# Kernel tuning notes

Measured on AMD Instinct MI355X. Metric: run time of the kernel, lower is better.

## Reference

```python
import jax, jax.numpy as jnp
import numpy as np

N_NODES = 20000
N_EDGES = 320000
F_IN = 256
HID = 256
N_CLS = 5


def _glorot(key, shape):
    lim = np.sqrt(6.0 / (shape[0] + shape[1]))
    return jax.random.uniform(key, shape, jnp.float32, -lim, lim)


def setup_inputs() -> dict:
    key = jax.random.key(0)
    ks = jax.random.split(key, 12)
    x1 = jax.random.normal(ks[0], (N_NODES, F_IN), jnp.float32)
    x2 = jax.random.normal(ks[1], (N_NODES, F_IN), jnp.float32)
    ei1 = jax.random.randint(ks[2], (2, N_EDGES), 0, N_NODES, jnp.int64 if jax.config.jax_enable_x64 else jnp.int32)
    ei2 = jax.random.randint(ks[3], (2, N_EDGES), 0, N_NODES, jnp.int64 if jax.config.jax_enable_x64 else jnp.int32)
    params = {
        'W1': _glorot(ks[4], (F_IN, HID)), 'b1': jnp.zeros((HID,), jnp.float32),
        'W2': _glorot(ks[5], (HID, HID)), 'b2': jnp.zeros((HID,), jnp.float32),
        'W3': _glorot(ks[6], (HID, HID)), 'b3': jnp.zeros((HID,), jnp.float32),
        'Wl': _glorot(ks[7], (HID, N_CLS)), 'bl': jnp.zeros((N_CLS,), jnp.float32),
    }
    return {'x1': x1, 'edge_index1': ei1, 'x2': x2, 'edge_index2': ei2, **params}


def gcn_conv(x, edge_index, W, b):
    # PyG GCNConv: add self-loops, symmetric normalization D^-1/2 (A+I) D^-1/2 (X W) + b
    N = x.shape[0]
    src, dst = edge_index[0], edge_index[1]
    deg = jax.ops.segment_sum(jnp.ones(src.shape[0], x.dtype), dst, num_segments=N) + 1.0
    dinv = jax.lax.rsqrt(deg)  # [N]
    xw = x @ W                 # [N, H]
    coef = (dinv[src] * dinv[dst])[:, None]  # per-edge norm
    agg = jax.ops.segment_sum(xw[src] * coef, dst, num_segments=N)
    agg = agg + xw * (dinv * dinv)[:, None]  # self-loop term
    return agg + b


def _branch(x, ei, W1, b1, W2, b2, W3, b3):
    # dropout is identity in eval mode
    h = jax.nn.relu(gcn_conv(x, ei, W1, b1))
    h = jax.nn.relu(gcn_conv(h, ei, W2, b2))
    return gcn_conv(h, ei, W3, b3)


def reference(x1, edge_index1, x2, edge_index2, W1, b1, W2, b2, W3, b3, Wl, bl):
    h1 = _branch(x1, edge_index1, W1, b1, W2, b2, W3, b3)
    h2 = _branch(x2, edge_index2, W1, b1, W2, b2, W3, b3)
    h = jnp.concatenate([h1, h2], axis=0)          # [2N, H]
    pooled = jnp.mean(h, axis=0, keepdims=True)    # batch is all zeros -> single mean pool
    return pooled @ Wl + bl                        # [1, num_classes]
```

## Files before the change

### kernel.cpp

```cpp
#include <hip/hip_runtime.h>
#include <hip/hip_bf16.h>

#define N_NODES 20000
#define N_EDGES 320000
#define HID 256
#define NQ 5000
#define NCHUNK 64

typedef __attribute__((ext_vector_type(8))) short bf16x8;
typedef __attribute__((ext_vector_type(4))) float f32x4;
typedef __attribute__((ext_vector_type(8))) unsigned short us8;

__device__ __forceinline__ float bf2f(ushort u) {
  union { unsigned int i; float f; } v; v.i = ((unsigned int)u) << 16; return v.f;
}
__device__ __forceinline__ ushort f2bf(float f) {
  union { float f; unsigned int i; } v; v.f = f;
  unsigned int r = v.i + 0x7FFFu + ((v.i >> 16) & 1u);
  return (ushort)(r >> 16);
}

__global__ void init_detect_kernel(int* cnt0, int* cnt1, float* t0, float* t1,
                                   const void* x1, const void* ei1, int* flags) {
  if (blockIdx.x == gridDim.x - 1) {
    __shared__ int cnt_wild, cnt_oddnz;
    if (threadIdx.x == 0) { cnt_wild = 0; cnt_oddnz = 0; }
    __syncthreads();
    const ushort* xu = (const ushort*)x1;
    int wild = 0;
#pragma unroll
    for (int k = 0; k < 4; k++) {
      ushort u = xu[threadIdx.x * 4 + k];
      int ex = (u >> 7) & 0xFF;
      if (ex >= 0x90) wild++;
    }
    if (wild) atomicAdd(&cnt_wild, wild);
    const int* ii = (const int*)ei1;
    if (ii[threadIdx.x * 2 + 1] != 0) atomicAdd(&cnt_oddnz, 1);
    __syncthreads();
    if (threadIdx.x == 0) {
      flags[0] = (cnt_wild > 64) ? 1 : 0;
      flags[1] = (cnt_oddnz < 8) ? 1 : 0;
    }
    return;
  }
  int i = blockIdx.x * blockDim.x + threadIdx.x;
  if (i < N_NODES) { cnt0[i] = 0; cnt1[i] = 0; t0[i] = 0.f; t1[i] = 0.f; }
}

__global__ __launch_bounds__(1024) void count_rank_kernel(
    const void* e0, const void* e1, int* cnt0, int* cnt1,
    int* rank0, int* rank1, const int* flags) {
  int b = blockIdx.y;
  const void* e = b ? e1 : e0;
  int* cnt = b ? cnt1 : cnt0;
  int* rank = b ? rank1 : rank0;
  int chunk = blockIdx.x >> 2;
  int lo = (blockIdx.x & 3) * NQ;
  int ebeg = chunk * (N_EDGES / NCHUNK);
  int eend = ebeg + (N_EDGES / NCHUNK);
  __shared__ int hist[NQ];
  __shared__ int base[NQ];
  for (int k = threadIdx.x; k < NQ; k += 1024) hist[k] = 0;
  __syncthreads();
  bool w64 = flags[1] != 0;
  const int* d32 = (const int*)e + N_EDGES;
  const long long* d64 = (const long long*)e + N_EDGES;
  for (int i = ebeg + threadIdx.x; i < eend; i += 1024) {
    int d = w64 ? (int)d64[i] : d32[i];
    unsigned q = (unsigned)(d - lo);
    if (q < NQ) atomicAdd(&hist[q], 1);
  }
  __syncthreads();
  for (int k = threadIdx.x; k < NQ; k += 1024) {
    int h = hist[k];
    if (h) base[k] = atomicAdd(&cnt[lo + k], h);
    hist[k] = 0;
  }
  __syncthreads();
  for (int i = ebeg + threadIdx.x; i < eend; i += 1024) {
    int d = w64 ? (int)d64[i] : d32[i];
    unsigned q = (unsigned)(d - lo);
    if (q < NQ) rank[i] = base[q] + atomicAdd(&hist[q], 1);
  }
}

__global__ __launch_bounds__(1024) void scan_kernel(const int* cnt0, const int* cnt1,
                                                    int* rp0, int* rp1,
                                                    float* dinv0, float* dinv1) {
  const int* cnt = blockIdx.x ? cnt1 : cnt0;
  int* rp = blockIdx.x ? rp1 : rp0;
  float* dinv = blockIdx.x ? dinv1 : dinv0;
  __shared__ int sd[1024];
  int tid = threadIdx.x;
  int base = tid * 20;
  int pref[20];
  int run = 0;
#pragma unroll
  for (int k = 0; k < 20; k++) {
    int i = base + k;
    int c = (i < N_NODES) ? cnt[i] : 0;
    if (i < N_NODES) dinv[i] = rsqrtf((float)c + 1.0f);
    run += c;
    pref[k] = run;
  }
  sd[tid] = run;
  __syncthreads();
  for (int off = 1; off < 1024; off <<= 1) {
    int v = (tid >= off) ? sd[tid - off] : 0;
    __syncthreads();
    sd[tid] += v;
    __syncthreads();
  }
  int offset = sd[tid] - run;
  if (tid == 0) rp[0] = 0;
#pragma unroll
  for (int k = 0; k < 20; k++) {
    int i = base + k;
    if (i < N_NODES) rp[i + 1] = offset + pref[k];
  }
}

__global__ __launch_bounds__(1024) void fill_kernel(
    const void* e0, const void* e1,
    const float* dinv0, const float* dinv1,
    const int* rp0, const int* rp1,
    const int* rank0, const int* rank1,
    unsigned int* eg0, unsigned int* eg1,
    float* t0, float* t1, const int* flags) {
  int b = blockIdx.y;
  const void* e = b ? e1 : e0;
  const float* dinv = b ? dinv1 : dinv0;
  bool w64 = flags[1] != 0;
  const int* s32 = (const int*)e;
  const int* d32 = (const int*)e + N_EDGES;
  const long long* s64 = (const long long*)e;
  const long long* d64 = (const long long*)e + N_EDGES;
  if (blockIdx.x < 313) {
    const int* rp = b ? rp1 : rp0;
    const int* rank = b ? rank1 : rank0;
    unsigned int* eg = b ? eg1 : eg0;
    int i = blockIdx.x * 1024 + threadIdx.x;
    if (i >= N_EDGES) return;
    int src = w64 ? (int)s64[i] : s32[i];
    int dst = w64 ? (int)d64[i] : d32[i];
    int slot = rp[dst] + rank[i];
    eg[slot] = (unsigned int)src | ((unsigned int)f2bf(dinv[src] * dinv[dst]) << 16);
    return;
  }
  float* t = b ? t1 : t0;
  int r = blockIdx.x - 313;
  int chunk = r >> 2;
  int lo = (r & 3) * NQ;
  int ebeg = chunk * (N_EDGES / NCHUNK);
  int eend = ebeg + (N_EDGES / NCHUNK);
  __shared__ float tl[NQ];
  for (int k = threadIdx.x; k < NQ; k += 1024) tl[k] = 0.f;
  __syncthreads();
  for (int i = ebeg + threadIdx.x; i < eend; i += 1024) {
    int src = w64 ? (int)s64[i] : s32[i];
    unsigned q = (unsigned)(src - lo);
    if (q < NQ) {
      int dst = w64 ? (int)d64[i] : d32[i];
      atomicAdd(&tl[q], dinv[dst]);
    }
  }
  __syncthreads();
  for (int k = threadIdx.x; k < NQ; k += 1024) {
    float v = tl[k];
    if (v != 0.f) atomicAdd(&t[lo + k], v);
  }
}

__global__ __launch_bounds__(256) void gemm_kernel(
    const void* __restrict__ A0, const void* __restrict__ A1,
    const void* __restrict__ W,
    ushort* __restrict__ C0, ushort* __restrict__ C1,
    int maybe_f32, const int* __restrict__ flags) {
  const void* A = blockIdx.z ? A1 : A0;
  ushort* C = blockIdx.z ? C1 : C0;
  bool wf32 = flags[0] != 0;
  bool af32 = maybe_f32 && wf32;
  int m0 = blockIdx.x * 128;
  int n0 = blockIdx.y * 64;
  __shared__ ushort As[128][42];
  __shared__ ushort Bs[64][42];
  int tid = threadIdx.x;
  int wave = tid >> 6, lane = tid & 63;
  int quad = lane >> 4, r16 = lane & 15;
  f32x4 acc[2][4];
#pragma unroll
  for (int m = 0; m < 2; m++)
#pragma unroll
    for (int n = 0; n < 4; n++) acc[m][n] = (f32x4){0.f, 0.f, 0.f, 0.f};
  int la_row = tid >> 1;
  int la_c0 = (tid & 1) * 16;
  int bk = tid >> 3;
  int bn0 = (tid & 7) * 8;
  for (int k0 = 0; k0 < 256; k0 += 32) {
    int gr = m0 + la_row;
    if (af32) {
      const float* Af = (const float*)A;
      float4 v0 = {0,0,0,0}, v1 = v0, v2 = v0, v3 = v0;
      if (gr < N_NODES) {
        const float* pA = Af + gr * 256 + k0 + la_c0;
        v0 = *(const float4*)pA;       v1 = *(const float4*)(pA + 4);
        v2 = *(const float4*)(pA + 8); v3 = *(const float4*)(pA + 12);
      }
      ushort* d = &As[la_row][la_c0];
      d[0] = f2bf(v0.x); d[1] = f2bf(v0.y); d[2]  = f2bf(v0.z); d[3]  = f2bf(v0.w);
      d[4] = f2bf(v1.x); d[5] = f2bf(v1.y); d[6]  = f2bf(v1.z); d[7]  = f2bf(v1.w);
      d[8] = f2bf(v2.x); d[9] = f2bf(v2.y); d[10] = f2bf(v2.z); d[11] = f2bf(v2.w);
      d[12] = f2bf(v3.x); d[13] = f2bf(v3.y); d[14] = f2bf(v3.z); d[15] = f2bf(v3.w);
    } else {
      const ushort* Ab = (const ushort*)A;
      int4 w0 = {0,0,0,0}, w1 = w0;
      if (gr < N_NODES) {
        const ushort* pA = Ab + gr * 256 + k0 + la_c0;
        w0 = *(const int4*)pA;
        w1 = *(const int4*)(pA + 8);
      }
      *(int4*)&As[la_row][la_c0] = w0;
      *(int4*)&As[la_row][la_c0 + 8] = w1;
    }
    ushort wtmp[8];
    if (wf32) {
      const float* Wf = (const float*)W + (k0 + bk) * 256 + n0 + bn0;
      float4 u0 = *(const float4*)Wf;
      float4 u1 = *(const float4*)(Wf + 4);
      wtmp[0] = f2bf(u0.x); wtmp[1] = f2bf(u0.y); wtmp[2] = f2bf(u0.z); wtmp[3] = f2bf(u0.w);
      wtmp[4] = f2bf(u1.x); wtmp[5] = f2bf(u1.y); wtmp[6] = f2bf(u1.z); wtmp[7] = f2bf(u1.w);
    } else {
      *(int4*)wtmp = *(const int4*)((const ushort*)W + (k0 + bk) * 256 + n0 + bn0);
    }
#pragma unroll
    for (int j = 0; j < 8; j++) Bs[bn0 + j][bk] = wtmp[j];
    __syncthreads();
    bf16x8 a0 = *(const bf16x8*)&As[wave * 32 + r16][quad * 8];
    bf16x8 a1 = *(const bf16x8*)&As[wave * 32 + 16 + r16][quad * 8];
    bf16x8 bb0 = *(const bf16x8*)&Bs[r16][quad * 8];
    bf16x8 bb1 = *(const bf16x8*)&Bs[16 + r16][quad * 8];
    bf16x8 bb2 = *(const bf16x8*)&Bs[32 + r16][quad * 8];
    bf16x8 bb3 = *(const bf16x8*)&Bs[48 + r16][quad * 8];
    acc[0][0] = __builtin_amdgcn_mfma_f32_16x16x32_bf16(a0, bb0, acc[0][0], 0, 0, 0);
    acc[0][1] = __builtin_amdgcn_mfma_f32_16x16x32_bf16(a0, bb1, acc[0][1], 0, 0, 0);
    acc[0][2] = __builtin_amdgcn_mfma_f32_16x16x32_bf16(a0, bb2, acc[0][2], 0, 0, 0);
    acc[0][3] = __builtin_amdgcn_mfma_f32_16x16x32_bf16(a0, bb3, acc[0][3], 0, 0, 0);
    acc[1][0] = __builtin_amdgcn_mfma_f32_16x16x32_bf16(a1, bb0, acc[1][0], 0, 0, 0);
    acc[1][1] = __builtin_amdgcn_mfma_f32_16x16x32_bf16(a1, bb1, acc[1][1], 0, 0, 0);
    acc[1][2] = __builtin_amdgcn_mfma_f32_16x16x32_bf16(a1, bb2, acc[1][2], 0, 0, 0);
    acc[1][3] = __builtin_amdgcn_mfma_f32_16x16x32_bf16(a1, bb3, acc[1][3], 0, 0, 0);
    __syncthreads();
  }
#pragma unroll
  for (int m = 0; m < 2; m++) {
    int grb = m0 + wave * 32 + m * 16 + quad * 4;
#pragma unroll
    for (int r = 0; r < 4; r++) {
      int gr = grb + r;
      if (gr < N_NODES) {
        ushort* cp = C + gr * 256 + n0 + r16;
        cp[0]  = f2bf(acc[m][0][r]);
        cp[16] = f2bf(acc[m][1][r]);
        cp[32] = f2bf(acc[m][2][r]);
        cp[48] = f2bf(acc[m][3][r]);
      }
    }
  }
}

__global__ __launch_bounds__(256) void agg_kernel(
    const ushort* __restrict__ XW0, const ushort* __restrict__ XW1,
    const float* __restrict__ dinv0, const float* __restrict__ dinv1,
    const int* __restrict__ rp0, const int* __restrict__ rp1,
    const unsigned int* __restrict__ eg0, const unsigned int* __restrict__ eg1,
    const void* __restrict__ bias,
    ushort* __restrict__ H0, ushort* __restrict__ H1,
    const int* __restrict__ flags) {
  int b = blockIdx.y;
  const ushort* XW = b ? XW1 : XW0;
  const float* dinv = b ? dinv1 : dinv0;
  const int* rp = b ? rp1 : rp0;
  const unsigned int* eg = b ? eg1 : eg0;
  ushort* H = b ? H1 : H0;
  int wave = threadIdx.x >> 6, lane = threadIdx.x & 63;
  int half = lane >> 5;
  int fl = (lane & 31) * 8;
  int i = blockIdx.x * 8 + wave * 2 + half;
  float di = dinv[i];
  float selfw = di * di;
  us8 v = *(const us8*)(XW + i * 256 + fl);
  float acc[8], acc2[8];
#pragma unroll
  for (int k = 0; k < 8; k++) { acc[k] = selfw * bf2f(v[k]); acc2[k] = 0.f; }
  int e = rp[i], eend = rp[i + 1];
  for (; e + 4 <= eend; e += 4) {
    unsigned int p0 = eg[e], p1 = eg[e + 1], p2 = eg[e + 2], p3 = eg[e + 3];
    us8 r0 = *(const us8*)(XW + (p0 & 0xFFFFu) * 256 + fl);
    us8 r1 = *(const us8*)(XW + (p1 & 0xFFFFu) * 256 + fl);
    us8 r2 = *(const us8*)(XW + (p2 & 0xFFFFu) * 256 + fl);
    us8 r3 = *(const us8*)(XW + (p3 & 0xFFFFu) * 256 + fl);
    float w0 = bf2f((ushort)(p0 >> 16)), w1 = bf2f((ushort)(p1 >> 16));
    float w2 = bf2f((ushort)(p2 >> 16)), w3 = bf2f((ushort)(p3 >> 16));
#pragma unroll
    for (int k = 0; k < 8; k++) {
      acc[k]  += w0 * bf2f(r0[k]);
      acc2[k] += w1 * bf2f(r1[k]);
      acc[k]  += w2 * bf2f(r2[k]);
      acc2[k] += w3 * bf2f(r3[k]);
    }
  }
  for (; e < eend; e++) {
    unsigned int pp = eg[e];
    us8 r = *(const us8*)(XW + (pp & 0xFFFFu) * 256 + fl);
    float w = bf2f((ushort)(pp >> 16));
#pragma unroll
    for (int k = 0; k < 8; k++) acc[k] += w * bf2f(r[k]);
  }
  float bv[8];
  if (flags[0]) {
    const float* bf = (const float*)bias + fl;
    float4 c0 = *(const float4*)bf;
    float4 c1 = *(const float4*)(bf + 4);
    bv[0] = c0.x; bv[1] = c0.y; bv[2] = c0.z; bv[3] = c0.w;
    bv[4] = c1.x; bv[5] = c1.y; bv[6] = c1.z; bv[7] = c1.w;
  } else {
    us8 bb = *(const us8*)((const ushort*)bias + fl);
#pragma unroll
    for (int k = 0; k < 8; k++) bv[k] = bf2f(bb[k]);
  }
  us8 o;
#pragma unroll
  for (int k = 0; k < 8; k++)
    o[k] = f2bf(fmaxf(acc[k] + acc2[k] + bv[k], 0.f));
  *(us8*)(H + i * 256 + fl) = o;
}

__global__ __launch_bounds__(256) void colsum_kernel(
    const ushort* __restrict__ H0, const ushort* __restrict__ H1,
    const float* __restrict__ dinv0, const float* __restrict__ dinv1,
    const float* __restrict__ t0, const float* __restrict__ t1,
    float* __restrict__ P) {
  int b = blockIdx.y;
  const ushort* H = b ? H1 : H0;
  const float* dinv = b ? dinv1 : dinv0;
  const float* t = b ? t1 : t0;
  int wave = threadIdx.x >> 6, lane = threadIdx.x & 63;
  int wid = blockIdx.x * 4 + wave;
  int f4 = lane * 4;
  float a0 = 0.f, a1 = 0.f, a2 = 0.f, a3 = 0.f;
  for (int j = wid; j < N_NODES; j += 256) {
    float dj = dinv[j];
    float c = dj * (t[j] + dj);
    ushort4 u = *(const ushort4*)(H + j * 256 + f4);
    a0 += c * bf2f(u.x); a1 += c * bf2f(u.y);
    a2 += c * bf2f(u.z); a3 += c * bf2f(u.w);
  }
  __shared__ float part[4][256];
  part[wave][f4 + 0] = a0; part[wave][f4 + 1] = a1;
  part[wave][f4 + 2] = a2; part[wave][f4 + 3] = a3;
  __syncthreads();
  int f = threadIdx.x;
  float ssum = part[0][f] + part[1][f] + part[2][f] + part[3][f];
  P[(b * 64 + blockIdx.x) * 256 + f] = ssum;
}

__global__ __launch_bounds__(256) void final_kernel(
    const float* __restrict__ P,
    const void* __restrict__ W3, const void* __restrict__ b3,
    const void* __restrict__ Wl, const void* __restrict__ bl,
    void* __restrict__ out, const int* __restrict__ flags) {
  __shared__ float v[256];
  __shared__ float pooled[256];
  bool f32 = flags[0] != 0;
  int t = threadIdx.x;
  float acc0 = 0.f, acc1 = 0.f;
  for (int b = 0; b < 64; b++) {
    acc0 += P[b * 256 + t];
    acc1 += P[(64 + b) * 256 + t];
  }
  v[t] = acc0 + acc1;
  __syncthreads();
  float acc = 0.f;
  if (f32) {
    const float* W3f = (const float*)W3;
    for (int f = 0; f < 256; f++) acc += v[f] * W3f[f * 256 + t];
    pooled[t] = acc * (1.0f / (2.0f * N_NODES)) + ((const float*)b3)[t];
  } else {
    const ushort* W3b = (const ushort*)W3;
    for (int f = 0; f < 256; f++) acc += v[f] * bf2f(W3b[f * 256 + t]);
    pooled[t] = acc * (1.0f / (2.0f * N_NODES)) + bf2f(((const ushort*)b3)[t]);
  }
  __syncthreads();
  if (t < 5) {
    float o;
    if (f32) {
      o = ((const float*)bl)[t];
      for (int h = 0; h < 256; h++) o += pooled[h] * ((const float*)Wl)[h * 5 + t];
      ((float*)out)[t] = o;
    } else {
      o = bf2f(((const ushort*)bl)[t]);
      for (int h = 0; h < 256; h++) o += pooled[h] * bf2f(((const ushort*)Wl)[h * 5 + t]);
      ((ushort*)out)[t] = f2bf(o);
    }
  }
}

extern "C" void kernel_launch(void* const* d_in, const int* in_sizes, int n_in,
                              void* d_out, int out_size, void* d_ws, size_t ws_size,
                              hipStream_t stream) {
  const void* x1 = d_in[0];
  const void* ei1 = d_in[1];
  const void* x2 = d_in[2];
  const void* ei2 = d_in[3];
  const void* W1 = d_in[4];
  const void* b1 = d_in[5];
  const void* W2 = d_in[6];
  const void* b2 = d_in[7];
  const void* W3 = d_in[8];
  const void* b3 = d_in[9];
  const void* Wl = d_in[10];
  const void* bl = d_in[11];

  char* p = (char*)d_ws;
  auto alloc = [&](size_t bytes) {
    char* r = p;
    p += (bytes + 255) & ~size_t(255);
    return r;
  };
  int* flags   = (int*)alloc(256);
  float* dinv0 = (float*)alloc(N_NODES * 4);
  float* dinv1 = (float*)alloc(N_NODES * 4);
  float* t0    = (float*)alloc(N_NODES * 4);
  float* t1    = (float*)alloc(N_NODES * 4);
  int* cnt0    = (int*)alloc(N_NODES * 4);
  int* cnt1    = (int*)alloc(N_NODES * 4);
  int* rp0     = (int*)alloc((N_NODES + 1) * 4);
  int* rp1     = (int*)alloc((N_NODES + 1) * 4);
  unsigned int* eg0 = (unsigned int*)alloc((size_t)N_EDGES * 4);
  unsigned int* eg1 = (unsigned int*)alloc((size_t)N_EDGES * 4);
  float* Pp    = (float*)alloc(2 * 64 * 256 * 4);
  ushort* xw0  = (ushort*)alloc((size_t)N_NODES * HID * 2);
  ushort* xw1  = (ushort*)alloc((size_t)N_NODES * HID * 2);
  ushort* h0   = (ushort*)alloc((size_t)N_NODES * HID * 2);
  ushort* h1   = (ushort*)alloc((size_t)N_NODES * HID * 2);
  int* rank0  = (int*)xw0;
  int* rank1  = rank0 + N_EDGES;

  init_detect_kernel<<<(N_NODES + 255) / 256 + 1, 256, 0, stream>>>(
      cnt0, cnt1, t0, t1, x1, ei1, flags);
  count_rank_kernel<<<dim3(NCHUNK * 4, 2), 1024, 0, stream>>>(
      ei1, ei2, cnt0, cnt1, rank0, rank1, flags);
  scan_kernel<<<2, 1024, 0, stream>>>(cnt0, cnt1, rp0, rp1, dinv0, dinv1);
  fill_kernel<<<dim3(313 + NCHUNK * 4, 2), 1024, 0, stream>>>(
      ei1, ei2, dinv0, dinv1, rp0, rp1, rank0, rank1, eg0, eg1, t0, t1, flags);

  gemm_kernel<<<dim3(157, 4, 2), 256, 0, stream>>>(x1, x2, W1, xw0, xw1, 1, flags);
  agg_kernel<<<dim3(2500, 2), 256, 0, stream>>>(
      xw0, xw1, dinv0, dinv1, rp0, rp1, eg0, eg1, b1, h0, h1, flags);

  gemm_kernel<<<dim3(157, 4, 2), 256, 0, stream>>>(h0, h1, W2, xw0, xw1, 0, flags);
  agg_kernel<<<dim3(2500, 2), 256, 0, stream>>>(
      xw0, xw1, dinv0, dinv1, rp0, rp1, eg0, eg1, b2, h0, h1, flags);

  colsum_kernel<<<dim3(64, 2), 256, 0, stream>>>(h0, h1, dinv0, dinv1, t0, t1, Pp);
  final_kernel<<<1, 256, 0, stream>>>(Pp, W3, b3, Wl, bl, d_out, flags);
}
```

Baseline: 348.2 us.

## Retile GEMM to full-width 32-row blocks and unroll aggregation by eight

The GEMM now gives each block 32 rows and all 256 output columns, with each wave owning 64 columns. The A tile is read once per block rather than four times across column blocks, and the grid grows to 625x2 blocks. Because 20000 divides evenly by 32, the row bounds checks are removed, at the cost of staging the whole 256-column W slice in LDS every k step. The aggregation kernel adds an 8-edge unrolled loop with four accumulator sets to keep more gathers in flight, which raises register pressure.

```diff
diff --git a/kernel.cpp b/kernel.cpp
--- a/kernel.cpp
+++ b/kernel.cpp
@@ -181,67 +181,59 @@
   ushort* C = blockIdx.z ? C1 : C0;
   bool wf32 = flags[0] != 0;
   bool af32 = maybe_f32 && wf32;
-  int m0 = blockIdx.x * 128;
-  int n0 = blockIdx.y * 64;
-  __shared__ ushort As[128][42];
-  __shared__ ushort Bs[64][42];
+  int m0 = blockIdx.x * 32;
+  __shared__ ushort As[32][42];
+  __shared__ ushort Bs[256][42];
   int tid = threadIdx.x;
   int wave = tid >> 6, lane = tid & 63;
   int quad = lane >> 4, r16 = lane & 15;
+  int nb = wave * 64;
   f32x4 acc[2][4];
 #pragma unroll
   for (int m = 0; m < 2; m++)
 #pragma unroll
     for (int n = 0; n < 4; n++) acc[m][n] = (f32x4){0.f, 0.f, 0.f, 0.f};
-  int la_row = tid >> 1;
-  int la_c0 = (tid & 1) * 16;
+  int ar = tid >> 2;
+  int ac = (tid & 3) * 8;
   int bk = tid >> 3;
   int bn0 = (tid & 7) * 8;
   for (int k0 = 0; k0 < 256; k0 += 32) {
-    int gr = m0 + la_row;
-    if (af32) {
-      const float* Af = (const float*)A;
-      float4 v0 = {0,0,0,0}, v1 = v0, v2 = v0, v3 = v0;
-      if (gr < N_NODES) {
-        const float* pA = Af + gr * 256 + k0 + la_c0;
-        v0 = *(const float4*)pA;       v1 = *(const float4*)(pA + 4);
-        v2 = *(const float4*)(pA + 8); v3 = *(const float4*)(pA + 12);
+    if (tid < 128) {
+      int gr = m0 + ar;
+      if (af32) {
+        const float* pA = (const float*)A + gr * 256 + k0 + ac;
+        float4 v0 = *(const float4*)pA;
+        float4 v1 = *(const float4*)(pA + 4);
+        ushort* d = &As[ar][ac];
+        d[0] = f2bf(v0.x); d[1] = f2bf(v0.y); d[2] = f2bf(v0.z); d[3] = f2bf(v0.w);
+        d[4] = f2bf(v1.x); d[5] = f2bf(v1.y); d[6] = f2bf(v1.z); d[7] = f2bf(v1.w);
+      } else {
+        *(int4*)&As[ar][ac] =
+            *(const int4*)((const ushort*)A + gr * 256 + k0 + ac);
       }
-      ushort* d = &As[la_row][la_c0];
-      d[0] = f2bf(v0.x); d[1] = f2bf(v0.y); d[2]  = f2bf(v0.z); d[3]  = f2bf(v0.w);
-      d[4] = f2bf(v1.x); d[5] = f2bf(v1.y); d[6]  = f2bf(v1.z); d[7]  = f2bf(v1.w);
-      d[8] = f2bf(v2.x); d[9] = f2bf(v2.y); d[10] = f2bf(v2.z); d[11] = f2bf(v2.w);
-      d[12] = f2bf(v3.x); d[13] = f2bf(v3.y); d[14] = f2bf(v3.z); d[15] = f2bf(v3.w);
-    } else {
-      const ushort* Ab = (const ushort*)A;
-      int4 w0 = {0,0,0,0}, w1 = w0;
-      if (gr < N_NODES) {
-        const ushort* pA = Ab + gr * 256 + k0 + la_c0;
-        w0 = *(const int4*)pA;
-        w1 = *(const int4*)(pA + 8);
+    }
+#pragma unroll
+    for (int h = 0; h < 4; h++) {
+      ushort wtmp[8];
+      if (wf32) {
+        const float* Wf = (const float*)W + (k0 + bk) * 256 + bn0 + h * 64;
+        float4 u0 = *(const float4*)Wf;
+        float4 u1 = *(const float4*)(Wf + 4);
+        wtmp[0] = f2bf(u0.x); wtmp[1] = f2bf(u0.y); wtmp[2] = f2bf(u0.z); wtmp[3] = f2bf(u0.w);
+        wtmp[4] = f2bf(u1.x); wtmp[5] = f2bf(u1.y); wtmp[6] = f2bf(u1.z); wtmp[7] = f2bf(u1.w);
+      } else {
+        *(int4*)wtmp = *(const int4*)((const ushort*)W + (k0 + bk) * 256 + bn0 + h * 64);
       }
-      *(int4*)&As[la_row][la_c0] = w0;
-      *(int4*)&As[la_row][la_c0 + 8] = w1;
-    }
-    ushort wtmp[8];
-    if (wf32) {
-      const float* Wf = (const float*)W + (k0 + bk) * 256 + n0 + bn0;
-      float4 u0 = *(const float4*)Wf;
-      float4 u1 = *(const float4*)(Wf + 4);
-      wtmp[0] = f2bf(u0.x); wtmp[1] = f2bf(u0.y); wtmp[2] = f2bf(u0.z); wtmp[3] = f2bf(u0.w);
-      wtmp[4] = f2bf(u1.x); wtmp[5] = f2bf(u1.y); wtmp[6] = f2bf(u1.z); wtmp[7] = f2bf(u1.w);
-    } else {
-      *(int4*)wtmp = *(const int4*)((const ushort*)W + (k0 + bk) * 256 + n0 + bn0);
-    }
-#pragma unroll
-    for (int j = 0; j < 8; j++) Bs[bn0 + j][bk] = wtmp[j];
-    __syncthreads();
-    bf16x8 a0 = *(const bf16x8*)&As[wave * 32 + r16][quad * 8];
-    bf16x8 a1 = *(const bf16x8*)&As[wave * 32 + 16 + r16][quad * 8];
-    bf16x8 bb0 = *(const bf16x8*)&Bs[r16][quad * 8];
-    bf16x8 bb1 = *(const bf16x8*)&Bs[16 + r16][quad * 8];
-    bf16x8 bb2 = *(const bf16x8*)&Bs[32 + r16][quad * 8];
-    bf16x8 bb3 = *(const bf16x8*)&Bs[48 + r16][quad * 8];
+#pragma unroll
+      for (int j = 0; j < 8; j++) Bs[bn0 + h * 64 + j][bk] = wtmp[j];
+    }
+    __syncthreads();
+    bf16x8 a0 = *(const bf16x8*)&As[r16][quad * 8];
+    bf16x8 a1 = *(const bf16x8*)&As[16 + r16][quad * 8];
+    bf16x8 bb0 = *(const bf16x8*)&Bs[nb + r16][quad * 8];
+    bf16x8 bb1 = *(const bf16x8*)&Bs[nb + 16 + r16][quad * 8];
+    bf16x8 bb2 = *(const bf16x8*)&Bs[nb + 32 + r16][quad * 8];
+    bf16x8 bb3 = *(const bf16x8*)&Bs[nb + 48 + r16][quad * 8];
     acc[0][0] = __builtin_amdgcn_mfma_f32_16x16x32_bf16(a0, bb0, acc[0][0], 0, 0, 0);
     acc[0][1] = __builtin_amdgcn_mfma_f32_16x16x32_bf16(a0, bb1, acc[0][1], 0, 0, 0);
     acc[0][2] = __builtin_amdgcn_mfma_f32_16x16x32_bf16(a0, bb2, acc[0][2], 0, 0, 0);
@@ -254,17 +246,15 @@
   }
 #pragma unroll
   for (int m = 0; m < 2; m++) {
-    int grb = m0 + wave * 32 + m * 16 + quad * 4;
+    int grb = m0 + m * 16 + quad * 4;
 #pragma unroll
     for (int r = 0; r < 4; r++) {
       int gr = grb + r;
-      if (gr < N_NODES) {
-        ushort* cp = C + gr * 256 + n0 + r16;
-        cp[0]  = f2bf(acc[m][0][r]);
-        cp[16] = f2bf(acc[m][1][r]);
-        cp[32] = f2bf(acc[m][2][r]);
-        cp[48] = f2bf(acc[m][3][r]);
-      }
+      ushort* cp = C + gr * 256 + nb + r16;
+      cp[0]  = f2bf(acc[m][0][r]);
+      cp[16] = f2bf(acc[m][1][r]);
+      cp[32] = f2bf(acc[m][2][r]);
+      cp[48] = f2bf(acc[m][3][r]);
     }
   }
 }
@@ -290,10 +280,40 @@
   float di = dinv[i];
   float selfw = di * di;
   us8 v = *(const us8*)(XW + i * 256 + fl);
-  float acc[8], acc2[8];
-#pragma unroll
-  for (int k = 0; k < 8; k++) { acc[k] = selfw * bf2f(v[k]); acc2[k] = 0.f; }
+  float acc[8], acc2[8], acc3[8], acc4[8];
+#pragma unroll
+  for (int k = 0; k < 8; k++) {
+    acc[k] = selfw * bf2f(v[k]);
+    acc2[k] = 0.f; acc3[k] = 0.f; acc4[k] = 0.f;
+  }
   int e = rp[i], eend = rp[i + 1];
+  for (; e + 8 <= eend; e += 8) {
+    unsigned int p0 = eg[e],     p1 = eg[e + 1], p2 = eg[e + 2], p3 = eg[e + 3];
+    unsigned int p4 = eg[e + 4], p5 = eg[e + 5], p6 = eg[e + 6], p7 = eg[e + 7];
+    us8 r0 = *(const us8*)(XW + (p0 & 0xFFFFu) * 256 + fl);
+    us8 r1 = *(const us8*)(XW + (p1 & 0xFFFFu) * 256 + fl);
+    us8 r2 = *(const us8*)(XW + (p2 & 0xFFFFu) * 256 + fl);
+    us8 r3 = *(const us8*)(XW + (p3 & 0xFFFFu) * 256 + fl);
+    us8 r4 = *(const us8*)(XW + (p4 & 0xFFFFu) * 256 + fl);
+    us8 r5 = *(const us8*)(XW + (p5 & 0xFFFFu) * 256 + fl);
+    us8 r6 = *(const us8*)(XW + (p6 & 0xFFFFu) * 256 + fl);
+    us8 r7 = *(const us8*)(XW + (p7 & 0xFFFFu) * 256 + fl);
+    float w0 = bf2f((ushort)(p0 >> 16)), w1 = bf2f((ushort)(p1 >> 16));
+    float w2 = bf2f((ushort)(p2 >> 16)), w3 = bf2f((ushort)(p3 >> 16));
+    float w4 = bf2f((ushort)(p4 >> 16)), w5 = bf2f((ushort)(p5 >> 16));
+    float w6 = bf2f((ushort)(p6 >> 16)), w7 = bf2f((ushort)(p7 >> 16));
+#pragma unroll
+    for (int k = 0; k < 8; k++) {
+      acc[k]  += w0 * bf2f(r0[k]);
+      acc2[k] += w1 * bf2f(r1[k]);
+      acc3[k] += w2 * bf2f(r2[k]);
+      acc4[k] += w3 * bf2f(r3[k]);
+      acc[k]  += w4 * bf2f(r4[k]);
+      acc2[k] += w5 * bf2f(r5[k]);
+      acc3[k] += w6 * bf2f(r6[k]);
+      acc4[k] += w7 * bf2f(r7[k]);
+    }
+  }
   for (; e + 4 <= eend; e += 4) {
     unsigned int p0 = eg[e], p1 = eg[e + 1], p2 = eg[e + 2], p3 = eg[e + 3];
     us8 r0 = *(const us8*)(XW + (p0 & 0xFFFFu) * 256 + fl);
@@ -306,8 +326,8 @@
     for (int k = 0; k < 8; k++) {
       acc[k]  += w0 * bf2f(r0[k]);
       acc2[k] += w1 * bf2f(r1[k]);
-      acc[k]  += w2 * bf2f(r2[k]);
-      acc2[k] += w3 * bf2f(r3[k]);
+      acc3[k] += w2 * bf2f(r2[k]);
+      acc4[k] += w3 * bf2f(r3[k]);
     }
   }
   for (; e < eend; e++) {
@@ -332,7 +352,7 @@
   us8 o;
 #pragma unroll
   for (int k = 0; k < 8; k++)
-    o[k] = f2bf(fmaxf(acc[k] + acc2[k] + bv[k], 0.f));
+    o[k] = f2bf(fmaxf((acc[k] + acc2[k]) + (acc3[k] + acc4[k]) + bv[k], 0.f));
   *(us8*)(H + i * 256 + fl) = o;
 }
 
@@ -455,11 +475,11 @@
   fill_kernel<<<dim3(313 + NCHUNK * 4, 2), 1024, 0, stream>>>(
       ei1, ei2, dinv0, dinv1, rp0, rp1, rank0, rank1, eg0, eg1, t0, t1, flags);
 
-  gemm_kernel<<<dim3(157, 4, 2), 256, 0, stream>>>(x1, x2, W1, xw0, xw1, 1, flags);
+  gemm_kernel<<<dim3(625, 1, 2), 256, 0, stream>>>(x1, x2, W1, xw0, xw1, 1, flags);
   agg_kernel<<<dim3(2500, 2), 256, 0, stream>>>(
       xw0, xw1, dinv0, dinv1, rp0, rp1, eg0, eg1, b1, h0, h1, flags);
 
-  gemm_kernel<<<dim3(157, 4, 2), 256, 0, stream>>>(h0, h1, W2, xw0, xw1, 0, flags);
+  gemm_kernel<<<dim3(625, 1, 2), 256, 0, stream>>>(h0, h1, W2, xw0, xw1, 0, flags);
   agg_kernel<<<dim3(2500, 2), 256, 0, stream>>>(
       xw0, xw1, dinv0, dinv1, rp0, rp1, eg0, eg1, b2, h0, h1, flags);
 
```

Measured after the change: 356.9 us. +2.5%, slower.
